# Kernel tuning notes

Hardware: AMD Instinct MI355X
Metric: run time of the kernel (lower is better)

Reference implementation:

```python
import jax, jax.numpy as jnp
import numpy as np


def setup_inputs() -> dict:
    key = jax.random.key(0)
    pred = jax.random.normal(key, (16, 4, 768, 768), dtype=jnp.float32)
    return {"pred": pred}


def _largest_cc(mask):
    """Largest 4-connected component of a 2D boolean mask, as float32 0/1.

    Equivalent to scipy.ndimage.label (default 4-connectivity) followed by
    keeping the largest label. Uses min-label flood propagation: each
    foreground pixel starts with its raster index; iterated neighbor-min
    converges so every pixel holds its component's minimum pixel index
    (the 'root'). Ties in size resolve to the smallest root, which matches
    scipy's label-order tie-breaking (labels assigned in raster order).
    """
    H, W = mask.shape
    HW = H * W
    idx = jnp.arange(HW, dtype=jnp.int32).reshape(H, W)
    BIG = jnp.int32(HW)  # sentinel for background
    lbl0 = jnp.where(mask, idx, BIG)

    def body(carry):
        lbl, _ = carry
        p = jnp.pad(lbl, 1, constant_values=HW)
        nb = jnp.minimum(jnp.minimum(p[:-2, 1:-1], p[2:, 1:-1]),
                         jnp.minimum(p[1:-1, :-2], p[1:-1, 2:]))
        new = jnp.where(mask, jnp.minimum(lbl, nb), BIG)
        return new, jnp.any(new != lbl)

    lbl, _ = jax.lax.while_loop(lambda c: c[1], body, (lbl0, jnp.any(mask)))

    # component sizes keyed by root pixel index; background bucket = HW
    sizes = jax.ops.segment_sum(mask.ravel().astype(jnp.int32), lbl.ravel(),
                                num_segments=HW + 1)
    sizes = sizes.at[HW].set(0)
    root = jnp.argmax(sizes).astype(jnp.int32)
    return ((lbl == root) & mask).astype(jnp.float32)


def reference(pred):
    B, C, H, W = pred.shape
    labels = jnp.argmax(pred, axis=1)  # [B, H, W]
    cls = jnp.arange(1, C, dtype=labels.dtype)
    masks = labels[:, None, :, :] == cls[None, :, None, None]  # [B, C-1, H, W]
    comp = jax.vmap(_largest_cc)(masks.reshape(-1, H, W)).reshape(B, C - 1, H, W)
    bg = 1.0 - jnp.clip(comp.sum(axis=1), 0.0, 1.0)  # channel 0
    return jnp.concatenate([bg[:, None], comp], axis=1)
```

## Files before the change

### kernel.cpp

```cpp
#include <hip/hip_runtime.h>
#include <stdint.h>

#define BB 16
#define CC 4
#define HH 768
#define WW 768
#define HW (HH * WW)
#define NPIX (BB * HW)
#define NIMG (BB * (CC - 1))
#define BEST_STRIDE 16

#define SH 16
#define SW 64
#define SPIX (SH * SW)
#define SX (WW / SW)
#define SY (HH / SH)
#define SPI (SX * SY)
#define WPB 4
#define CCL_TPB (WPB * 64)

typedef unsigned long long ull;


__device__ __forceinline__ int find_root(int* P, int i) {
    int p = P[i];
    while (p != i) {
        int gp = P[p];
        P[i] = gp;
        i = p;
        p = gp;
    }
    return i;
}

__device__ __forceinline__ void merge(int* P, int a, int b) {
    a = find_root(P, a);
    b = find_root(P, b);
    while (a != b) {
        if (a < b) { int t = a; a = b; b = t; }
        int old = atomicCAS(&P[a], a, b);
        if (old == a) return;
        a = find_root(P, old);
        b = find_root(P, b);
    }
}


__device__ __forceinline__ int lfind(int* P, int i) {
    int p = P[i];
    while (p != i) {
        int gp = P[p];
        P[i] = gp;
        i = p;
        p = gp;
    }
    return i;
}

__device__ __forceinline__ void lmerge(int* P, int a, int b) {
    a = lfind(P, a);
    b = lfind(P, b);
    while (a != b) {
        if (a < b) { int t = a; a = b; b = t; }
        int old = atomicCAS(&P[a], a, b);
        if (old == a) return;
        a = lfind(P, old);
        b = lfind(P, b);
    }
}

__device__ __forceinline__ ull umax64(ull a, ull b) { return a > b ? a : b; }

__device__ __forceinline__ void lds_fence() {
    asm volatile("s_waitcnt lgkmcnt(0)" ::: "memory");
    __builtin_amdgcn_sched_barrier(0);
}


__global__ __launch_bounds__(CCL_TPB) void k_strip_ccl(
        const float* __restrict__ pred,
        uint8_t* __restrict__ labels,
        int* __restrict__ parent,
        uint32_t* __restrict__ counts,
        ull* __restrict__ best) {
    __shared__ __align__(16) int sp_all[WPB][SPIX];

    if (blockIdx.x == 0) {
        for (int i = threadIdx.x; i < NIMG * BEST_STRIDE; i += CCL_TPB) best[i] = 0ull;
    }

    const int tid = (int)threadIdx.x;
    const int w = tid >> 6;
    const int lane = tid & 63;
    int* sp = sp_all[w];

    const int gs = blockIdx.x * WPB + w;
    const int img = gs / SPI;
    const int s = gs % SPI;
    const int tr = (s / SX) * SH;
    const int tc = (s % SX) * SW;
    const float* pb = pred + (size_t)img * CC * HW;
    const int imgbase = img * HW;
    const int col0 = tr * WW + tc + lane;

    int lab[SH];
    int v[SH];

    #pragma unroll
    for (int r = 0; r < SH; ++r) {
        int gi = col0 + r * WW;
        float b0 = pb[gi];
        float b1 = pb[gi + HW];
        float b2 = pb[gi + 2 * HW];
        float b3 = pb[gi + 3 * HW];
        int l = 0;
        float bv = b0;
        if (b1 > bv) { bv = b1; l = 1; }
        if (b2 > bv) { bv = b2; l = 2; }
        if (b3 > bv) { bv = b3; l = 3; }
        lab[r] = l;
        labels[imgbase + gi] = (uint8_t)l;
    }

    #pragma unroll
    for (int r = 0; r < SH; ++r) {
        int l = lab[r];
        int labL = __shfl_up(l, 1, 64);
        bool isStart = l && (lane == 0 || labL != l);
        ull mask = __ballot(isStart);
        int li = (r << 6) + lane;
        int vr = li;
        if (l) {
            ull mle = mask & (~0ull >> (63 - lane));
            vr = (r << 6) + (63 - __clzll(mle));
        }
        v[r] = vr;
        sp[li] = vr;
    }
    lds_fence();

    #pragma unroll
    for (int r = 1; r < SH; ++r) {
        int l = lab[r];
        int lU = lab[r - 1];
        int labL = __shfl_up(l, 1, 64);
        int labUL = __shfl_up(lU, 1, 64);
        if (l && lU == l) {
            if (lane == 0 || !(labL == l && labUL == l))
                lmerge(sp, v[r], v[r - 1]);
        }
    }
    lds_fence();

    #pragma unroll
    for (int r = 0; r < SH; ++r) {
        int l = lab[r];
        int labL = __shfl_up(l, 1, 64);
        int labR = __shfl_down(l, 1, 64);
        bool isStart = l && (lane == 0 || labL != l);
        bool isEnd = l && (lane == 63 || labR != l);
        ull endmask = __ballot(isEnd);
        int li = (r << 6) + lane;
        if (l) {
            int p = sp[li] & 0xFFFF;
            if (p != li) {
                int q0 = sp[p] & 0xFFFF;
                while (q0 != p) { p = q0; q0 = sp[p] & 0xFFFF; }
                sp[li] = p;
            }
            if (isStart) {
                ull mge = endmask & (~0ull << lane);
                int epos = __ffsll((long long)mge) - 1;
                int runlen = epos - lane + 1;
                atomicAdd((unsigned int*)&sp[p], (unsigned int)runlen << 16);
            }
        }
    }
    lds_fence();

    #pragma unroll
    for (int r = 0; r < SH; ++r) {
        int li = (r << 6) + lane;
        int gi = imgbase + col0 + r * WW;
        int sv = sp[li];
        int root = sv & 0xFFFF;
        int pv = -1;
        uint32_t cv = 0u;
        if (lab[r]) {
            pv = imgbase + (tr + (root >> 6)) * WW + tc + (root & 63);
            cv = (root == li) ? ((uint32_t)sv >> 16) : 0u;
        }
        parent[gi] = pv;
        counts[gi] = cv;
    }
}

#define VED ((SX - 1) * HH)
#define HED ((SY - 1) * WW)
#define EPI (VED + HED)
__global__ void k_border_merge(const uint8_t* __restrict__ labels, int* parent) {
    int t = blockIdx.x * blockDim.x + threadIdx.x;
    if (t >= BB * EPI) return;
    int img = t / EPI;
    int e = t % EPI;
    int a, b;
    if (e < VED) {
        int j = e / HH, r = e % HH;
        int c = (j + 1) * SW - 1;
        a = r * WW + c;
        b = a + 1;
    } else {
        e -= VED;
        int j = e / WW, c = e % WW;
        int r = (j + 1) * SH - 1;
        a = r * WW + c;
        b = a + WW;
    }
    int ga = img * HW + a, gb = img * HW + b;
    uint8_t la = labels[ga];
    if (la && labels[gb] == la) merge(parent, ga, gb);
}

__global__ void k_compress(int* __restrict__ parent, uint32_t* __restrict__ counts) {
    int q = blockIdx.x * blockDim.x + threadIdx.x;
    if (q >= NPIX / 4) return;
    int t = q * 4;
    uint4 cv = *(const uint4*)&counts[t];
    if (!(cv.x | cv.y | cv.z | cv.w)) return;
    uint32_t cs[4] = {cv.x, cv.y, cv.z, cv.w};
    #pragma unroll
    for (int j = 0; j < 4; ++j) {
        if (!cs[j]) continue;
        int i = t + j;
        int g = parent[i];
        if (g == i) continue;
        while (true) { int pg = parent[g]; if (pg == g) break; g = pg; }
        parent[i] = g;
        atomicAdd(&counts[g], cs[j]);
        counts[i] = 0;
    }
}

#define BEST_BLK_PER_IMG 144
#define BEST_TPB 256
#define BEST_PIX_PER_BLK (HW / BEST_BLK_PER_IMG)
__global__ void k_best(const uint8_t* __restrict__ labels,
                       const uint32_t* __restrict__ counts,
                       ull* __restrict__ best) {
    __shared__ ull sw[(BEST_TPB / 64) * 3];
    int img = blockIdx.x / BEST_BLK_PER_IMG;
    int chunk = blockIdx.x % BEST_BLK_PER_IMG;
    int base = img * HW + chunk * BEST_PIX_PER_BLK;

    ull l0 = 0, l1 = 0, l2 = 0;
    for (int k = 0; k < BEST_PIX_PER_BLK; k += BEST_TPB * 4) {
        int t = base + k + (int)threadIdx.x * 4;
        uint4 cv = *(const uint4*)&counts[t];
        if (cv.x | cv.y | cv.z | cv.w) {
            uchar4 lv = *(const uchar4*)&labels[t];
            uint32_t cs[4] = {cv.x, cv.y, cv.z, cv.w};
            uint8_t ls[4] = {lv.x, lv.y, lv.z, lv.w};
            #pragma unroll
            for (int j = 0; j < 4; ++j) {
                if (cs[j]) {
                    int cc = (int)ls[j] - 1;
                    ull key = ((ull)cs[j] << 32) | (ull)(~(uint32_t)(t + j));
                    if (cc == 0) l0 = umax64(l0, key);
                    else if (cc == 1) l1 = umax64(l1, key);
                    else l2 = umax64(l2, key);
                }
            }
        }
    }
    #pragma unroll
    for (int m = 1; m < 64; m <<= 1) {
        l0 = umax64(l0, __shfl_xor(l0, m, 64));
        l1 = umax64(l1, __shfl_xor(l1, m, 64));
        l2 = umax64(l2, __shfl_xor(l2, m, 64));
    }
    int lane = threadIdx.x & 63;
    int wid = threadIdx.x >> 6;
    if (lane == 0) { sw[wid * 3 + 0] = l0; sw[wid * 3 + 1] = l1; sw[wid * 3 + 2] = l2; }
    __syncthreads();
    if (threadIdx.x < 3) {
        ull m = 0;
        for (int w = 0; w < BEST_TPB / 64; ++w) m = umax64(m, sw[w * 3 + threadIdx.x]);
        if (m) atomicMax(&best[(img * 3 + (int)threadIdx.x) * BEST_STRIDE], m);
    }
}

__global__ void k_output(const uint8_t* __restrict__ labels,
                         const int* __restrict__ parent,
                         const ull* __restrict__ best,
                         float* __restrict__ out) {
    int q = blockIdx.x * blockDim.x + threadIdx.x;
    if (q >= NPIX / 4) return;
    int t = q * 4;
    int b = t / HW;
    int i = t - b * HW;
    uchar4 lv = *(const uchar4*)&labels[t];
    int4 pv = *(const int4*)&parent[t];
    int root[3];
    root[0] = (int)(~(uint32_t)best[(b * 3 + 0) * BEST_STRIDE]);
    root[1] = (int)(~(uint32_t)best[(b * 3 + 1) * BEST_STRIDE]);
    root[2] = (int)(~(uint32_t)best[(b * 3 + 2) * BEST_STRIDE]);

    uint8_t ls[4] = {lv.x, lv.y, lv.z, lv.w};
    int ps[4] = {pv.x, pv.y, pv.z, pv.w};
    float fg[4];
    #pragma unroll
    for (int j = 0; j < 4; ++j) {
        int g = -1;
        if (ps[j] >= 0) g = parent[ps[j]];
        fg[j] = (ls[j] && g == root[ls[j] - 1]) ? 1.0f : 0.0f;
    }

    float4 o0, o1, o2, o3;
    float* c0 = &o0.x; float* c1 = &o1.x; float* c2 = &o2.x; float* c3 = &o3.x;
    #pragma unroll
    for (int j = 0; j < 4; ++j) {
        c0[j] = 1.0f - fg[j];
        c1[j] = (ls[j] == 1) ? fg[j] : 0.0f;
        c2[j] = (ls[j] == 2) ? fg[j] : 0.0f;
        c3[j] = (ls[j] == 3) ? fg[j] : 0.0f;
    }
    float* o = out + (size_t)b * CC * HW + i;
    *(float4*)&o[0] = o0;
    *(float4*)&o[HW] = o1;
    *(float4*)&o[2 * HW] = o2;
    *(float4*)&o[3 * HW] = o3;
}


extern "C" void kernel_launch(void* const* d_in, const int* in_sizes, int n_in,
                              void* d_out, int out_size, void* d_ws, size_t ws_size,
                              hipStream_t stream) {
    const float* pred = (const float*)d_in[0];
    float* out = (float*)d_out;

    uint8_t* labels = (uint8_t*)d_ws;
    int* parent = (int*)((char*)d_ws + NPIX);
    ull* best = (ull*)((char*)d_ws + NPIX + (size_t)NPIX * 4);
    uint32_t* counts = (uint32_t*)d_out;

    const int TPB = 256;

    k_strip_ccl<<<BB * SPI / WPB, CCL_TPB, 0, stream>>>(pred, labels, parent, counts, best);
    k_border_merge<<<(BB * EPI + TPB - 1) / TPB, TPB, 0, stream>>>(labels, parent);
    k_compress<<<(NPIX / 4 + TPB - 1) / TPB, TPB, 0, stream>>>(parent, counts);
    k_best<<<BB * BEST_BLK_PER_IMG, BEST_TPB, 0, stream>>>(labels, counts, best);
    k_output<<<(NPIX / 4 + TPB - 1) / TPB, TPB, 0, stream>>>(labels, parent, best, out);
}
```

Measured before the change: 154.7 us.

## Halve strip height, batch pred loads, pack class id into root counts

Strip height drops from 16 to 8 rows, which doubles the number of strips and the border edges that must be merged. All pred loads for a strip are now issued before the argmax so more memory requests are in flight at once. The class id is packed into the low two bits of each root's count, so k_best no longer reads the labels array. The packing requires counts to stay below 2^30, and the extra border-merge work is a possible cost.

```diff
diff --git a/kernel.cpp b/kernel.cpp
--- a/kernel.cpp
+++ b/kernel.cpp
@@ -10,7 +10,7 @@
 #define NIMG (BB * (CC - 1))
 #define BEST_STRIDE 16
 
-#define SH 16
+#define SH 8
 #define SW 64
 #define SPIX (SH * SW)
 #define SX (WW / SW)
@@ -106,20 +106,24 @@
     int lab[SH];
     int v[SH];
 
+    float b0[SH], b1[SH], b2[SH], b3[SH];
     #pragma unroll
     for (int r = 0; r < SH; ++r) {
         int gi = col0 + r * WW;
-        float b0 = pb[gi];
-        float b1 = pb[gi + HW];
-        float b2 = pb[gi + 2 * HW];
-        float b3 = pb[gi + 3 * HW];
+        b0[r] = pb[gi];
+        b1[r] = pb[gi + HW];
+        b2[r] = pb[gi + 2 * HW];
+        b3[r] = pb[gi + 3 * HW];
+    }
+    #pragma unroll
+    for (int r = 0; r < SH; ++r) {
         int l = 0;
-        float bv = b0;
-        if (b1 > bv) { bv = b1; l = 1; }
-        if (b2 > bv) { bv = b2; l = 2; }
-        if (b3 > bv) { bv = b3; l = 3; }
+        float bv = b0[r];
+        if (b1[r] > bv) { bv = b1[r]; l = 1; }
+        if (b2[r] > bv) { bv = b2[r]; l = 2; }
+        if (b3[r] > bv) { bv = b3[r]; l = 3; }
         lab[r] = l;
-        labels[imgbase + gi] = (uint8_t)l;
+        labels[imgbase + col0 + r * WW] = (uint8_t)l;
     }
 
     #pragma unroll
@@ -188,7 +192,7 @@
         uint32_t cv = 0u;
         if (lab[r]) {
             pv = imgbase + (tr + (root >> 6)) * WW + tc + (root & 63);
-            cv = (root == li) ? ((uint32_t)sv >> 16) : 0u;
+            cv = (root == li) ? ((((uint32_t)sv >> 16) << 2) | (uint32_t)(lab[r] - 1)) : 0u;
         }
         parent[gi] = pv;
         counts[gi] = cv;
@@ -236,7 +240,7 @@
         if (g == i) continue;
         while (true) { int pg = parent[g]; if (pg == g) break; g = pg; }
         parent[i] = g;
-        atomicAdd(&counts[g], cs[j]);
+        atomicAdd(&counts[g], cs[j] & ~3u);
         counts[i] = 0;
     }
 }
@@ -244,8 +248,7 @@
 #define BEST_BLK_PER_IMG 144
 #define BEST_TPB 256
 #define BEST_PIX_PER_BLK (HW / BEST_BLK_PER_IMG)
-__global__ void k_best(const uint8_t* __restrict__ labels,
-                       const uint32_t* __restrict__ counts,
+__global__ void k_best(const uint32_t* __restrict__ counts,
                        ull* __restrict__ best) {
     __shared__ ull sw[(BEST_TPB / 64) * 3];
     int img = blockIdx.x / BEST_BLK_PER_IMG;
@@ -257,14 +260,13 @@
         int t = base + k + (int)threadIdx.x * 4;
         uint4 cv = *(const uint4*)&counts[t];
         if (cv.x | cv.y | cv.z | cv.w) {
-            uchar4 lv = *(const uchar4*)&labels[t];
             uint32_t cs[4] = {cv.x, cv.y, cv.z, cv.w};
-            uint8_t ls[4] = {lv.x, lv.y, lv.z, lv.w};
             #pragma unroll
             for (int j = 0; j < 4; ++j) {
-                if (cs[j]) {
-                    int cc = (int)ls[j] - 1;
-                    ull key = ((ull)cs[j] << 32) | (ull)(~(uint32_t)(t + j));
+                uint32_t raw = cs[j];
+                if (raw) {
+                    int cc = (int)(raw & 3u);
+                    ull key = ((ull)(raw >> 2) << 32) | (ull)(~(uint32_t)(t + j));
                     if (cc == 0) l0 = umax64(l0, key);
                     else if (cc == 1) l1 = umax64(l1, key);
                     else l2 = umax64(l2, key);
@@ -348,6 +350,6 @@
     k_strip_ccl<<<BB * SPI / WPB, CCL_TPB, 0, stream>>>(pred, labels, parent, counts, best);
     k_border_merge<<<(BB * EPI + TPB - 1) / TPB, TPB, 0, stream>>>(labels, parent);
     k_compress<<<(NPIX / 4 + TPB - 1) / TPB, TPB, 0, stream>>>(parent, counts);
-    k_best<<<BB * BEST_BLK_PER_IMG, BEST_TPB, 0, stream>>>(labels, counts, best);
+    k_best<<<BB * BEST_BLK_PER_IMG, BEST_TPB, 0, stream>>>(counts, best);
     k_output<<<(NPIX / 4 + TPB - 1) / TPB, TPB, 0, stream>>>(labels, parent, best, out);
 }
```

Measured after the change: 146.6 us. 1.06x faster.
